# Kernel tuning notes

Measured on AMD Instinct MI355X. Metric: run time of the kernel, lower is better.

Reference implementation:

```python
import jax, jax.numpy as jnp
import numpy as np

B, N = 16, 4096
NPOINT, RADIUS, NSAMPLE = 1024, 0.2, 64
IN_CH = 9
MLP = [64, 64, 128]
EPS = 1e-5  # torch BatchNorm2d default eps


def setup_inputs() -> dict:
    key = jax.random.key(0)
    ks = jax.random.split(key, 2 + 4 * len(MLP))
    inp = {
        'xyz': jax.random.uniform(ks[0], (B, N, 3), jnp.float32),
        'points': jax.random.normal(ks[1], (B, N, 6), jnp.float32),
    }
    last = IN_CH
    for i, oc in enumerate(MLP):
        k = 2 + 4 * i
        inp[f'w{i}'] = jax.random.normal(ks[k], (oc, last), jnp.float32) * (1.0 / np.sqrt(last))
        inp[f'b{i}'] = jnp.zeros((oc,), jnp.float32)
        inp[f'g{i}'] = jnp.ones((oc,), jnp.float32)
        inp[f'be{i}'] = jnp.zeros((oc,), jnp.float32)
        last = oc
    return inp


def _gather(feat, idx):
    # feat [B, N, C], idx [B, ...] int -> [B, ..., C]
    return jax.vmap(lambda f, i: f[i])(feat, idx)


def _fps(xyz, npoint):
    # furthest point sampling, CUDA-kernel semantics: start at index 0.
    b, n, _ = xyz.shape

    def step(carry, _):
        dist, far = carry  # dist [B,N], far [B]
        centroid = _gather(xyz, far)  # [B,3]
        d = jnp.sum((xyz - centroid[:, None, :]) ** 2, axis=-1)  # [B,N]
        dist = jnp.minimum(dist, d)
        return (dist, jnp.argmax(dist, axis=1).astype(jnp.int32)), far

    init = (jnp.full((b, n), 1e10, xyz.dtype), jnp.zeros((b,), jnp.int32))
    _, idx = jax.lax.scan(step, init, None, length=npoint)
    return idx.T  # [B, npoint]


def _ball_query(radius, nsample, xyz, new_xyz):
    # idx [B, S, nsample]; first-found padding like the CUDA kernel.
    n = xyz.shape[1]
    # squared distances via gemm to avoid a [B,S,N,3] broadcast temp
    sqr = (jnp.sum(new_xyz ** 2, -1)[:, :, None]
           + jnp.sum(xyz ** 2, -1)[:, None, :]
           - 2.0 * jnp.einsum('bsc,bnc->bsn', new_xyz, xyz))  # [B,S,N]
    gidx = jnp.where(sqr > radius * radius, n, jnp.arange(n, dtype=jnp.int32)[None, None, :])
    gidx = jnp.sort(gidx, axis=-1)[:, :, :nsample]
    first = gidx[:, :, :1]  # centers are sampled points -> always valid
    return jnp.where(gidx == n, first, gidx)


def _forward(xyz, points, params):
    fps_idx = jax.lax.stop_gradient(_fps(xyz, NPOINT))
    new_xyz = _gather(xyz, fps_idx)  # [B,S,3]
    idx = _ball_query(RADIUS, NSAMPLE, xyz, new_xyz)  # [B,S,K]
    grouped_xyz = _gather(xyz, idx) - new_xyz[:, :, None, :]  # [B,S,K,3]
    grouped_pts = _gather(points, idx)  # [B,S,K,D]
    x = jnp.concatenate([grouped_xyz, grouped_pts], axis=-1)  # [B,S,K,C]
    for w, b, g, be in params:
        x = jnp.einsum('bskc,oc->bsko', x, w) + b  # 1x1 conv
        m = jnp.mean(x, axis=(0, 1, 2))
        v = jnp.var(x, axis=(0, 1, 2))  # biased var, as torch BN training mode
        x = jax.nn.relu(g * (x - m) * jax.lax.rsqrt(v + EPS) + be)
    new_points = jnp.max(x, axis=2).transpose(0, 2, 1)  # [B, C_out, S]
    return new_xyz, new_points


def reference(xyz, points, w0, b0, g0, be0, w1, b1, g1, be1, w2, b2, g2, be2):
    params = [(w0, b0, g0, be0), (w1, b1, g1, be1), (w2, b2, g2, be2)]
    return _forward(xyz, points, params)
```

## Files before the change

### kernel.cpp

```cpp
#include <hip/hip_runtime.h>
#include <hip/hip_bf16.h>
#include <stdint.h>

#define NBATCH 16
#define NPTS   4096
#define NPT    1024
#define NSMP   64
#define R2     0.04f
#define ICH    9
#define OC1    64
#define OC2    64
#define OC3    128
#define NROWS  (NBATCH*NPT*NSMP)
#define NBLK1  (NROWS/256)
#define NBLK23 (NROWS/128)
#define NTOTF  1048576.0f

typedef __attribute__((ext_vector_type(8))) short short8;
typedef __attribute__((ext_vector_type(4))) float f32x4;
typedef __attribute__((ext_vector_type(2))) float f32x2;

__device__ __forceinline__ short f2bf(float f) {
    __hip_bfloat16 h = __float2bfloat16(f);
    return *reinterpret_cast<short*>(&h);
}

#define DPP32_MAXF(v, CTRL, RM) do {                                         \
    int _mv = __builtin_amdgcn_update_dpp(__float_as_int(v),                 \
                                          __float_as_int(v),                 \
                                          CTRL, RM, 0xF, false);             \
    (v) = fmaxf((v), __int_as_float(_mv));                                   \
} while (0)

__global__ __launch_bounds__(256) void k_fps(const float* __restrict__ xyz,
                                             float* __restrict__ newxyz)
{
    const int b   = blockIdx.x;
    const int tid = threadIdx.x;
    const float* X = xyz + (size_t)b * NPTS * 3;

    __shared__ __align__(16) float sxyz[NPTS * 4];
    __shared__ float scf[NPT * 3];
    __shared__ float sVal[4];
    __shared__ unsigned sIdx[2];

    f32x2 px[8], py[8], pz[8], dd[8];
#pragma unroll
    for (int m = 0; m < 8; ++m) {
        int p0 = tid + (2*m+0) * 256;
        int p1 = tid + (2*m+1) * 256;
        float x0 = X[p0*3+0], y0 = X[p0*3+1], z0 = X[p0*3+2];
        float x1 = X[p1*3+0], y1 = X[p1*3+1], z1 = X[p1*3+2];
        px[m] = (f32x2){x0, x1}; py[m] = (f32x2){y0, y1}; pz[m] = (f32x2){z0, z1};
        sxyz[p0*4+0] = x0; sxyz[p0*4+1] = y0; sxyz[p0*4+2] = z0;
        sxyz[p1*4+0] = x1; sxyz[p1*4+1] = y1; sxyz[p1*4+2] = z1;
        dd[m] = (f32x2){1e10f, 1e10f};
    }
    if (tid == 0) { sIdx[0] = 0u; sIdx[1] = 0u; }
    __syncthreads();

    float cx = sxyz[0], cy = sxyz[1], cz = sxyz[2];

    for (int it = 0; it < NPT; ++it) {
        const int buf = it & 1;
        if (tid == 0) {
            scf[it*3+0] = cx; scf[it*3+1] = cy; scf[it*3+2] = cz;
        }
        const f32x2 c2x = (f32x2){cx, cx};
        const f32x2 c2y = (f32x2){cy, cy};
        const f32x2 c2z = (f32x2){cz, cz};
#pragma unroll
        for (int m = 0; m < 8; ++m) {
            f32x2 dx = px[m] - c2x, dy = py[m] - c2y, dz = pz[m] - c2z;
            f32x2 d  = dx*dx + dy*dy + dz*dz;
            dd[m] = __builtin_elementwise_min(dd[m], d);
        }
        f32x2 t0 = __builtin_elementwise_max(dd[0], dd[1]);
        f32x2 t1 = __builtin_elementwise_max(dd[2], dd[3]);
        f32x2 t2 = __builtin_elementwise_max(dd[4], dd[5]);
        f32x2 t3 = __builtin_elementwise_max(dd[6], dd[7]);
        f32x2 u0 = __builtin_elementwise_max(t0, t1);
        f32x2 u1 = __builtin_elementwise_max(t2, t3);
        f32x2 v  = __builtin_elementwise_max(u0, u1);
        const float lmax = fmaxf(v.x, v.y);

        float wmax = lmax;
        DPP32_MAXF(wmax, 0x111, 0xF);
        DPP32_MAXF(wmax, 0x112, 0xF);
        DPP32_MAXF(wmax, 0x114, 0xF);
        DPP32_MAXF(wmax, 0x118, 0xF);
        DPP32_MAXF(wmax, 0x142, 0xA);
        DPP32_MAXF(wmax, 0x143, 0xC);
        if ((tid & 63) == 63) sVal[tid >> 6] = wmax;
        __syncthreads();

        const float gmax = fmaxf(fmaxf(sVal[0], sVal[1]),
                                 fmaxf(sVal[2], sVal[3]));

        if (lmax == gmax) {
            unsigned cand = 0u;
#pragma unroll
            for (int m = 0; m < 8; ++m) {
                if (dd[m].x == gmax)
                    cand = max(cand, 0xFFFFFFFFu - (unsigned)(tid + (2*m+0)*256));
                if (dd[m].y == gmax)
                    cand = max(cand, 0xFFFFFFFFu - (unsigned)(tid + (2*m+1)*256));
            }
            atomicMax(&sIdx[buf], cand);
        }
        __syncthreads();

        const int far = (int)(0xFFFFFFFFu - sIdx[buf]);
        if (tid == 0) sIdx[buf ^ 1] = 0u;
        const f32x4 c4 = *(const f32x4*)&sxyz[far*4];
        cx = c4.x; cy = c4.y; cz = c4.z;
    }

    __syncthreads();
    float* outb = newxyz + (size_t)b * NPT * 3;
    for (int i = tid; i < NPT*3; i += 256) outb[i] = scf[i];
}

__global__ __launch_bounds__(256) void k_ballq(const float* __restrict__ xyz,
                                               const float* __restrict__ pts,
                                               const float* __restrict__ newxyz,
                                               float* __restrict__ x0)
{
    const int wave = threadIdx.x >> 6;
    const int lane = threadIdx.x & 63;
    const int g = blockIdx.x * 4 + wave;
    const int b = g >> 10;
    const float* X = xyz + (size_t)b * NPTS * 3;
    const float* P = pts + (size_t)b * NPTS * 6;
    const float cx = newxyz[(size_t)g*3+0];
    const float cy = newxyz[(size_t)g*3+1];
    const float cz = newxyz[(size_t)g*3+2];
    const float sn = cx*cx + cy*cy + cz*cz;

    __shared__ int sFirst[4];
    int total = 0;
    for (int chunk = 0; chunk < NPTS/64; ++chunk) {
        int p = chunk*64 + lane;
        float x = X[p*3+0], y = X[p*3+1], z = X[p*3+2];
        float sp  = x*x + y*y + z*z;
        float dot = cx*x + cy*y + cz*z;
        float sqr = (sn + sp) - 2.0f*dot;
        bool inb = !(sqr > R2);
        unsigned long long mask = __ballot(inb);
        int before = __popcll(mask & ((1ull << lane) - 1ull));
        int pos = total + before;
        if (inb && pos < NSMP) {
            if (pos == 0) sFirst[wave] = p;
            float* row = x0 + ((size_t)g * NSMP + pos) * ICH;
            row[0] = x - cx; row[1] = y - cy; row[2] = z - cz;
#pragma unroll
            for (int c = 0; c < 6; ++c) row[3+c] = P[(size_t)p*6 + c];
        }
        total += (int)__popcll(mask);
        if (total >= NSMP) break;
    }
    if (total < NSMP) {
        int first = sFirst[wave];
        float x = X[first*3+0], y = X[first*3+1], z = X[first*3+2];
        float r0 = x - cx, r1 = y - cy, r2 = z - cz;
        float q0 = P[(size_t)first*6+0], q1 = P[(size_t)first*6+1], q2 = P[(size_t)first*6+2];
        float q3 = P[(size_t)first*6+3], q4 = P[(size_t)first*6+4], q5 = P[(size_t)first*6+5];
        for (int slot = total + lane; slot < NSMP; slot += 64) {
            float* row = x0 + ((size_t)g * NSMP + slot) * ICH;
            row[0]=r0; row[1]=r1; row[2]=r2;
            row[3]=q0; row[4]=q1; row[5]=q2; row[6]=q3; row[7]=q4; row[8]=q5;
        }
    }
}

__global__ __launch_bounds__(256) void k_prep(const float* __restrict__ w1,
                                              const float* __restrict__ w2,
                                              short* __restrict__ w1f,
                                              short* __restrict__ w2f)
{
    int t = blockIdx.x * 256 + threadIdx.x;
    if (t < 8*64) {
        int f = t >> 6, l = t & 63;
        int n = f >> 1, kb = f & 1;
        int col = n*16 + (l & 15);
        int k0  = kb*32 + (l >> 4)*8;
#pragma unroll
        for (int j = 0; j < 8; ++j)
            w1f[((size_t)t)*8 + j] = f2bf(w1[col*64 + k0 + j]);
    } else if (t < 8*64 + 16*64) {
        int t2 = t - 8*64;
        int f = t2 >> 6, l = t2 & 63;
        int n = f >> 1, kb = f & 1;
        int col = n*16 + (l & 15);
        int k0  = kb*32 + (l >> 4)*8;
#pragma unroll
        for (int j = 0; j < 8; ++j)
            w2f[((size_t)t2)*8 + j] = f2bf(w2[col*64 + k0 + j]);
    }
}

__global__ __launch_bounds__(256) void k_mlp1(
    const float* __restrict__ x0,
    const float* __restrict__ w0, const float* __restrict__ b0,
    float* __restrict__ pSum, float* __restrict__ pSq)
{
    __shared__ float staged[32 * 256];
    const int tid = threadIdx.x;
    const int bid = blockIdx.x;
    const size_t row = (size_t)bid * 256 + tid;

    float x[ICH];
    const float* xr = x0 + row * ICH;
#pragma unroll
    for (int c = 0; c < ICH; ++c) x[c] = xr[c];

    float h1[OC1];
#pragma unroll
    for (int o = 0; o < OC1; ++o) {
        float a = b0[o];
#pragma unroll
        for (int c = 0; c < ICH; ++c) a += w0[o*ICH + c] * x[c];
        h1[o] = a;
    }
#pragma unroll
    for (int cb = 0; cb < OC1; cb += 32) {
        __syncthreads();
#pragma unroll
        for (int o = 0; o < 32; ++o) staged[o*256 + tid] = h1[cb + o];
        __syncthreads();
        const int ch = tid >> 3, seg = tid & 7;
        const float* col = staged + ch*256 + seg*32;
        float s1 = 0.f, s2 = 0.f;
#pragma unroll
        for (int i = 0; i < 32; ++i) {
            float vv = col[(i + tid) & 31];
            s1 += vv; s2 += vv*vv;
        }
#pragma unroll
        for (int m = 1; m < 8; m <<= 1) {
            s1 += __shfl_xor(s1, m, 64);
            s2 += __shfl_xor(s2, m, 64);
        }
        if (seg == 0) {
            pSum[(size_t)bid*OC1 + cb + ch] = s1;
            pSq [(size_t)bid*OC1 + cb + ch] = s2;
        }
    }
}

template<int DEPTH>
__global__ __launch_bounds__(256) void k_mlp23(
    const float* __restrict__ x0,
    const float* __restrict__ w0, const float* __restrict__ b0,
    const short* __restrict__ w1f, const float* __restrict__ b1,
    const short* __restrict__ w2f, const float* __restrict__ b2,
    const float* __restrict__ AC,
    float* __restrict__ pSum, float* __restrict__ pSq,
    float* __restrict__ maxk)
{
    __shared__ __align__(16) short h1s[128*64];
    __shared__ __align__(16) short h2s[128*64];
    __shared__ __align__(16) short w1s[8*64*8];
    __shared__ __align__(16) short w2s[16*64*8];
    __shared__ float sS[4][128];
    __shared__ float sQ[4][128];
    __shared__ float sM[4][128];

    const int tid = threadIdx.x;
    const int bid = blockIdx.x;

    {
        const uint4* s1 = (const uint4*)w1f;
        uint4* d1 = (uint4*)w1s;
        for (int i = tid; i < 512; i += 256) d1[i] = s1[i];
        if (DEPTH == 3) {
            const uint4* s2 = (const uint4*)w2f;
            uint4* d2 = (uint4*)w2s;
            for (int i = tid; i < 1024; i += 256) d2[i] = s2[i];
        }
    }

    {
        const int rloc = tid & 127;
        const int half = __builtin_amdgcn_readfirstlane(tid >> 7);
        const size_t rowg = (size_t)bid * 128 + rloc;
        const float* xr = x0 + rowg * ICH;
        float x[ICH];
#pragma unroll
        for (int c = 0; c < ICH; ++c) x[c] = xr[c];
        const float* w0h = w0 + half*32*ICH;
        const float* b0h = b0 + half*32;
        const float* Ah  = AC + half*32;
        const float* Ch  = AC + 64 + half*32;
        float h[32];
#pragma unroll
        for (int o = 0; o < 32; ++o) {
            float a = b0h[o];
#pragma unroll
            for (int c = 0; c < ICH; ++c) a += w0h[o*ICH + c] * x[c];
            h[o] = fmaxf(Ah[o]*a + Ch[o], 0.0f);
        }
#pragma unroll
        for (int q = 0; q < 4; ++q) {
            short8 v;
#pragma unroll
            for (int j = 0; j < 8; ++j) v[j] = f2bf(h[q*8 + j]);
            int byte = (rloc*128 + half*64 + q*16) ^ ((rloc & 7) << 4);
            *(short8*)((char*)h1s + byte) = v;
        }
    }
    __syncthreads();

    const int wv = tid >> 6;
    const int l  = tid & 63;
    const int lr = l & 15, lk = l >> 4;

    f32x4 acc2[2][4];
    const f32x4 fz = {0.f, 0.f, 0.f, 0.f};
#pragma unroll
    for (int m = 0; m < 2; ++m)
#pragma unroll
        for (int n = 0; n < 4; ++n) acc2[m][n] = fz;

    short8 afr[2][2];
#pragma unroll
    for (int m = 0; m < 2; ++m)
#pragma unroll
        for (int kb = 0; kb < 2; ++kb) {
            int row = wv*32 + m*16 + lr;
            int byte = (row*128 + (kb*4 + lk)*16) ^ ((row & 7) << 4);
            afr[m][kb] = *(short8*)((char*)h1s + byte);
        }
#pragma unroll
    for (int n = 0; n < 4; ++n) {
        short8 bf0 = *(short8*)(w1s + ((n*2+0)*64 + l)*8);
        short8 bf1 = *(short8*)(w1s + ((n*2+1)*64 + l)*8);
#pragma unroll
        for (int m = 0; m < 2; ++m) {
            acc2[m][n] = __builtin_amdgcn_mfma_f32_16x16x32_bf16(afr[m][0], bf0, acc2[m][n], 0, 0, 0);
            acc2[m][n] = __builtin_amdgcn_mfma_f32_16x16x32_bf16(afr[m][1], bf1, acc2[m][n], 0, 0, 0);
        }
    }
#pragma unroll
    for (int n = 0; n < 4; ++n) {
        float bb = b1[n*16 + lr];
#pragma unroll
        for (int m = 0; m < 2; ++m)
#pragma unroll
            for (int r = 0; r < 4; ++r) acc2[m][n][r] += bb;
    }

    if (DEPTH == 2) {
#pragma unroll
        for (int n = 0; n < 4; ++n) {
            float s1 = 0.f, s2 = 0.f;
#pragma unroll
            for (int m = 0; m < 2; ++m)
#pragma unroll
                for (int r = 0; r < 4; ++r) {
                    float v = acc2[m][n][r];
                    s1 += v; s2 += v*v;
                }
            s1 += __shfl_xor(s1, 16, 64); s1 += __shfl_xor(s1, 32, 64);
            s2 += __shfl_xor(s2, 16, 64); s2 += __shfl_xor(s2, 32, 64);
            if (l < 16) { sS[wv][n*16 + l] = s1; sQ[wv][n*16 + l] = s2; }
        }
        __syncthreads();
        if (tid < OC2) {
            float a = 0.f, q = 0.f;
#pragma unroll
            for (int w = 0; w < 4; ++w) { a += sS[w][tid]; q += sQ[w][tid]; }
            pSum[(size_t)bid*OC2 + tid] = a;
            pSq [(size_t)bid*OC2 + tid] = q;
        }
        return;
    }

#pragma unroll
    for (int n = 0; n < 4; ++n) {
        int c = n*16 + lr;
        float A2 = AC[128 + c], C2 = AC[192 + c];
#pragma unroll
        for (int m = 0; m < 2; ++m)
#pragma unroll
            for (int r = 0; r < 4; ++r) {
                float v = fmaxf(A2*acc2[m][n][r] + C2, 0.0f);
                int row = wv*32 + m*16 + lk*4 + r;
                int byte = (row*128 + c*2) ^ ((row & 7) << 4);
                *(short*)((char*)h2s + byte) = f2bf(v);
            }
    }
    __syncthreads();

    f32x4 acc3[2][8];
#pragma unroll
    for (int m = 0; m < 2; ++m)
#pragma unroll
        for (int n = 0; n < 8; ++n) acc3[m][n] = fz;

    short8 afr2[2][2];
#pragma unroll
    for (int m = 0; m < 2; ++m)
#pragma unroll
        for (int kb = 0; kb < 2; ++kb) {
            int row = wv*32 + m*16 + lr;
            int byte = (row*128 + (kb*4 + lk)*16) ^ ((row & 7) << 4);
            afr2[m][kb] = *(short8*)((char*)h2s + byte);
        }
#pragma unroll
    for (int n = 0; n < 8; ++n) {
        short8 bf0 = *(short8*)(w2s + ((n*2+0)*64 + l)*8);
        short8 bf1 = *(short8*)(w2s + ((n*2+1)*64 + l)*8);
#pragma unroll
        for (int m = 0; m < 2; ++m) {
            acc3[m][n] = __builtin_amdgcn_mfma_f32_16x16x32_bf16(afr2[m][0], bf0, acc3[m][n], 0, 0, 0);
            acc3[m][n] = __builtin_amdgcn_mfma_f32_16x16x32_bf16(afr2[m][1], bf1, acc3[m][n], 0, 0, 0);
        }
    }

#pragma unroll
    for (int n = 0; n < 8; ++n) {
        float bb = b2[n*16 + lr];
        float s1 = 0.f, s2 = 0.f, mx = -3.0e38f;
#pragma unroll
        for (int m = 0; m < 2; ++m)
#pragma unroll
            for (int r = 0; r < 4; ++r) {
                float v = acc3[m][n][r] + bb;
                s1 += v; s2 += v*v; mx = fmaxf(mx, v);
            }
        s1 += __shfl_xor(s1, 16, 64); s1 += __shfl_xor(s1, 32, 64);
        s2 += __shfl_xor(s2, 16, 64); s2 += __shfl_xor(s2, 32, 64);
        mx = fmaxf(mx, __shfl_xor(mx, 16, 64));
        mx = fmaxf(mx, __shfl_xor(mx, 32, 64));
        if (l < 16) {
            sS[wv][n*16 + l] = s1;
            sQ[wv][n*16 + l] = s2;
            sM[wv][n*16 + l] = mx;
        }
    }
    __syncthreads();
    if (tid < OC3) {
        float a = 0.f, q = 0.f;
#pragma unroll
        for (int w = 0; w < 4; ++w) { a += sS[w][tid]; q += sQ[w][tid]; }
        pSum[(size_t)bid*OC3 + tid] = a;
        pSq [(size_t)bid*OC3 + tid] = q;
    }
    {
        int g = tid >> 7, c = tid & 127;
        maxk[((size_t)bid*2 + g)*OC3 + c] = fmaxf(sM[2*g][c], sM[2*g+1][c]);
    }
}

__global__ __launch_bounds__(256) void k_finalize(
    const float* __restrict__ pSum, const float* __restrict__ pSq,
    const float* __restrict__ g, const float* __restrict__ be,
    float* __restrict__ A, float* __restrict__ C, int OC, int nblk)
{
    const int o = blockIdx.x, tid = threadIdx.x;
    float s1 = 0.f, s2 = 0.f;
    for (int i = tid; i < nblk; i += 256) {
        s1 += pSum[(size_t)i*OC + o];
        s2 += pSq [(size_t)i*OC + o];
    }
    __shared__ float r1[256], r2[256];
    r1[tid] = s1; r2[tid] = s2;
    __syncthreads();
    for (int s = 128; s > 0; s >>= 1) {
        if (tid < s) { r1[tid] += r1[tid+s]; r2[tid] += r2[tid+s]; }
        __syncthreads();
    }
    if (tid == 0) {
        float mean = r1[0] * (1.0f / NTOTF);
        float var  = r2[0] * (1.0f / NTOTF) - mean*mean;
        float a = g[o] / sqrtf(var + 1e-5f);
        A[o] = a;
        C[o] = be[o] - mean * a;
    }
}

__global__ __launch_bounds__(256) void k_out(const float* __restrict__ maxk,
                                             const float* __restrict__ A,
                                             const float* __restrict__ C,
                                             float* __restrict__ out1)
{
    int idx = blockIdx.x * 256 + threadIdx.x;
    int s  = idx & (NPT - 1);
    int ch = (idx >> 10) & (OC3 - 1);
    int b  = idx >> 17;
    float v = maxk[((size_t)(b * NPT + s)) * OC3 + ch];
    out1[idx] = fmaxf(A[ch] * v + C[ch], 0.0f);
}

extern "C" void kernel_launch(void* const* d_in, const int* in_sizes, int n_in,
                              void* d_out, int out_size, void* d_ws, size_t ws_size,
                              hipStream_t stream)
{
    const float* xyz = (const float*)d_in[0];
    const float* pts = (const float*)d_in[1];
    const float* w0  = (const float*)d_in[2];
    const float* b0  = (const float*)d_in[3];
    const float* g0  = (const float*)d_in[4];
    const float* be0 = (const float*)d_in[5];
    const float* w1  = (const float*)d_in[6];
    const float* b1  = (const float*)d_in[7];
    const float* g1  = (const float*)d_in[8];
    const float* be1 = (const float*)d_in[9];
    const float* w2  = (const float*)d_in[10];
    const float* b2  = (const float*)d_in[11];
    const float* g2  = (const float*)d_in[12];
    const float* be2 = (const float*)d_in[13];

    float* out0 = (float*)d_out;
    float* out1 = out0 + (size_t)NBATCH*NPT*3;

    float* ws   = (float*)d_ws;
    float* x0   = ws;
    float* pSum = x0   + (size_t)NROWS*ICH;
    float* pSq  = pSum + (size_t)NBLK23*OC3;
    float* AC   = pSq  + (size_t)NBLK23*OC3;
    float* maxk = AC + 512;
    short* w1f  = (short*)(maxk + (size_t)NBATCH*NPT*OC3);
    short* w2f  = w1f + 8*64*8;

    k_prep <<<6, 256, 0, stream>>>(w1, w2, w1f, w2f);
    k_fps  <<<NBATCH, 256, 0, stream>>>(xyz, out0);
    k_ballq<<<(NBATCH*NPT)/4, 256, 0, stream>>>(xyz, pts, out0, x0);

    k_mlp1<<<NBLK1, 256, 0, stream>>>(x0, w0, b0, pSum, pSq);
    k_finalize<<<OC1, 256, 0, stream>>>(pSum, pSq, g0, be0, AC+0,   AC+64,  OC1, NBLK1);
    k_mlp23<2><<<NBLK23, 256, 0, stream>>>(x0, w0,b0, w1f,b1, w2f,b2, AC, pSum, pSq, maxk);
    k_finalize<<<OC2, 256, 0, stream>>>(pSum, pSq, g1, be1, AC+128, AC+192, OC2, NBLK23);
    k_mlp23<3><<<NBLK23, 256, 0, stream>>>(x0, w0,b0, w1f,b1, w2f,b2, AC, pSum, pSq, maxk);
    k_finalize<<<OC3, 256, 0, stream>>>(pSum, pSq, g2, be2, AC+256, AC+384, OC3, NBLK23);

    k_out<<<(NBATCH*OC3*NPT)/256, 256, 0, stream>>>(maxk, AC+256, AC+384, out1);
}
```

Baseline: 1.089 ms.

## Pack FPS argmax into 64-bit keys and replace block barriers with flag spin

The FPS loop now packs each thread's max distance and its index into a single 64-bit key and reduces it with a DPP wave max. The per-iteration pair of __syncthreads plus the LDS atomicMax are replaced by per-wave keys and volatile tag counters that every thread spins on. Points are also assigned contiguously per thread (16 per thread) and loaded with vectorized float4 reads. This removes two barriers and the atomic from the serial 1024-step loop. In exchange it doubles the DPP traffic and relies on a correct double-buffered spin-wait ordering across waves without a full barrier.

```diff
diff --git a/kernel.cpp b/kernel.cpp
--- a/kernel.cpp
+++ b/kernel.cpp
@@ -25,38 +25,51 @@
     return *reinterpret_cast<short*>(&h);
 }
 
-#define DPP32_MAXF(v, CTRL, RM) do {                                         \
-    int _mv = __builtin_amdgcn_update_dpp(__float_as_int(v),                 \
-                                          __float_as_int(v),                 \
-                                          CTRL, RM, 0xF, false);             \
-    (v) = fmaxf((v), __int_as_float(_mv));                                   \
+#define DPP64_MAX(k, CTRL, RM) do {                                          \
+    unsigned _lo = (unsigned)(k); unsigned _hi = (unsigned)((k) >> 32);      \
+    unsigned _nlo = (unsigned)__builtin_amdgcn_update_dpp((int)_lo, (int)_lo,\
+                                                    CTRL, RM, 0xF, false);   \
+    unsigned _nhi = (unsigned)__builtin_amdgcn_update_dpp((int)_hi, (int)_hi,\
+                                                    CTRL, RM, 0xF, false);   \
+    unsigned long long _nk = ((unsigned long long)_nhi << 32) | _nlo;        \
+    if (_nk > (k)) (k) = _nk;                                                \
 } while (0)
 
 __global__ __launch_bounds__(256) void k_fps(const float* __restrict__ xyz,
                                              float* __restrict__ newxyz)
 {
-    const int b   = blockIdx.x;
-    const int tid = threadIdx.x;
+    const int b    = blockIdx.x;
+    const int tid  = threadIdx.x;
+    const int wv   = tid >> 6;
+    const int lane = tid & 63;
     const float* X = xyz + (size_t)b * NPTS * 3;
 
     __shared__ __align__(16) float sxyz[NPTS * 4];
     __shared__ float scf[NPT * 3];
-    __shared__ float sVal[4];
-    __shared__ unsigned sIdx[2];
-
+    __shared__ unsigned long long sKeyD[2][4];
+    __shared__ volatile unsigned sTag[4];
+
+    const int p0 = tid * 16;
     f32x2 px[8], py[8], pz[8], dd[8];
-#pragma unroll
-    for (int m = 0; m < 8; ++m) {
-        int p0 = tid + (2*m+0) * 256;
-        int p1 = tid + (2*m+1) * 256;
-        float x0 = X[p0*3+0], y0 = X[p0*3+1], z0 = X[p0*3+2];
-        float x1 = X[p1*3+0], y1 = X[p1*3+1], z1 = X[p1*3+2];
-        px[m] = (f32x2){x0, x1}; py[m] = (f32x2){y0, y1}; pz[m] = (f32x2){z0, z1};
-        sxyz[p0*4+0] = x0; sxyz[p0*4+1] = y0; sxyz[p0*4+2] = z0;
-        sxyz[p1*4+0] = x1; sxyz[p1*4+1] = y1; sxyz[p1*4+2] = z1;
-        dd[m] = (f32x2){1e10f, 1e10f};
-    }
-    if (tid == 0) { sIdx[0] = 0u; sIdx[1] = 0u; }
+    {
+        const f32x4* src = (const f32x4*)(X + (size_t)p0 * 3);
+        float c[48];
+#pragma unroll
+        for (int q = 0; q < 12; ++q) *(f32x4*)&c[q*4] = src[q];
+#pragma unroll
+        for (int m = 0; m < 8; ++m) {
+            px[m] = (f32x2){c[6*m+0], c[6*m+3]};
+            py[m] = (f32x2){c[6*m+1], c[6*m+4]};
+            pz[m] = (f32x2){c[6*m+2], c[6*m+5]};
+            dd[m] = (f32x2){1e10f, 1e10f};
+        }
+#pragma unroll
+        for (int j = 0; j < 16; ++j) {
+            *(f32x4*)&sxyz[(p0 + j) * 4] =
+                (f32x4){c[3*j+0], c[3*j+1], c[3*j+2], 0.f};
+        }
+    }
+    if (tid < 4) sTag[tid] = 0u;
     __syncthreads();
 
     float cx = sxyz[0], cy = sxyz[1], cz = sxyz[2];
@@ -83,35 +96,36 @@
         f32x2 u1 = __builtin_elementwise_max(t2, t3);
         f32x2 v  = __builtin_elementwise_max(u0, u1);
         const float lmax = fmaxf(v.x, v.y);
-
-        float wmax = lmax;
-        DPP32_MAXF(wmax, 0x111, 0xF);
-        DPP32_MAXF(wmax, 0x112, 0xF);
-        DPP32_MAXF(wmax, 0x114, 0xF);
-        DPP32_MAXF(wmax, 0x118, 0xF);
-        DPP32_MAXF(wmax, 0x142, 0xA);
-        DPP32_MAXF(wmax, 0x143, 0xC);
-        if ((tid & 63) == 63) sVal[tid >> 6] = wmax;
-        __syncthreads();
-
-        const float gmax = fmaxf(fmaxf(sVal[0], sVal[1]),
-                                 fmaxf(sVal[2], sVal[3]));
-
-        if (lmax == gmax) {
-            unsigned cand = 0u;
-#pragma unroll
-            for (int m = 0; m < 8; ++m) {
-                if (dd[m].x == gmax)
-                    cand = max(cand, 0xFFFFFFFFu - (unsigned)(tid + (2*m+0)*256));
-                if (dd[m].y == gmax)
-                    cand = max(cand, 0xFFFFFFFFu - (unsigned)(tid + (2*m+1)*256));
-            }
-            atomicMax(&sIdx[buf], cand);
-        }
-        __syncthreads();
-
-        const int far = (int)(0xFFFFFFFFu - sIdx[buf]);
-        if (tid == 0) sIdx[buf ^ 1] = 0u;
+        unsigned cand = 0u;
+#pragma unroll
+        for (int m = 7; m >= 0; --m) {
+            if (dd[m].y == lmax) cand = 0xFFFFFFFFu - (unsigned)(p0 + 2*m + 1);
+            if (dd[m].x == lmax) cand = 0xFFFFFFFFu - (unsigned)(p0 + 2*m + 0);
+        }
+        unsigned long long key =
+            ((unsigned long long)__float_as_uint(lmax) << 32) | cand;
+        DPP64_MAX(key, 0x111, 0xF);
+        DPP64_MAX(key, 0x112, 0xF);
+        DPP64_MAX(key, 0x114, 0xF);
+        DPP64_MAX(key, 0x118, 0xF);
+        DPP64_MAX(key, 0x142, 0xA);
+        DPP64_MAX(key, 0x143, 0xC);
+
+        if (lane == 63) sKeyD[buf][wv] = key;
+        __threadfence_block();
+        if (lane == 0) sTag[wv] = (unsigned)(it + 1);
+
+        const unsigned need = (unsigned)(it + 1);
+        for (;;) {
+            unsigned g0 = sTag[0], g1 = sTag[1], g2 = sTag[2], g3 = sTag[3];
+            if (g0 >= need && g1 >= need && g2 >= need && g3 >= need) break;
+        }
+        volatile unsigned long long* kp = sKeyD[buf];
+        unsigned long long k0 = kp[0], k1 = kp[1], k2 = kp[2], k3 = kp[3];
+        unsigned long long m01 = k0 > k1 ? k0 : k1;
+        unsigned long long m23 = k2 > k3 ? k2 : k3;
+        unsigned long long bb  = m01 > m23 ? m01 : m23;
+        const int far = (int)(0xFFFFFFFFu - (unsigned)(bb & 0xFFFFFFFFull));
         const f32x4 c4 = *(const f32x4*)&sxyz[far*4];
         cx = c4.x; cy = c4.y; cz = c4.z;
     }
```

Result: slower. 1.197 ms (+10.0%).
